# Kernel tuning notes

Measured on AMD Instinct MI355X. Metric: run time of the kernel, lower is better.

Reference implementation:

```python
import jax, jax.numpy as jnp
import numpy as np

K = 20  # kNN fan-out


def knn_idx(x, k):
    # x: (B, C, N). Negative squared pairwise distance; top-k largest = nearest.
    inner = -2.0 * jnp.einsum('bcn,bcm->bnm', x, x)        # (B, N, N)
    xx = jnp.sum(x * x, axis=1)                            # (B, N)
    pd = -xx[:, :, None] - inner - xx[:, None, :]          # (B, N, N)
    return jax.lax.top_k(pd, k)[1]                         # (B, N, k) int32


def get_graph_feature(x, k):
    # x: (B, C, N) -> edge features (B, 2C, N, k)
    idx = knn_idx(x, k)                                    # (B, N, k)
    xt = jnp.transpose(x, (0, 2, 1))                       # (B, N, C)
    nbrs = jax.vmap(lambda pts, ids: pts[ids])(xt, idx)    # (B, N, k, C)
    center = xt[:, :, None, :]                             # (B, N, 1, C)
    feat = jnp.concatenate(
        [nbrs - center, jnp.broadcast_to(center, nbrs.shape)], axis=-1)  # (B,N,k,2C)
    return jnp.transpose(feat, (0, 3, 1, 2))               # (B, 2C, N, k)


def vn_layer(W, x):
    # W: (out, in); x: (B, in, N, k) -> (B, out, N, k)
    return jnp.einsum('oi,bink->bonk', W, x)


def setup_inputs() -> dict:
    key = jax.random.key(0)
    ks = jax.random.split(key, 6)
    B, C, N = 16, 3, 2048
    num_classes = 10
    return {
        'x': jax.random.normal(ks[0], (B, C, N), dtype=jnp.float32),
        'W1': jax.random.normal(ks[1], (64, 6), dtype=jnp.float32),
        'W2': jax.random.normal(ks[2], (128, 64), dtype=jnp.float32),
        'W3': jax.random.normal(ks[3], (256, 128), dtype=jnp.float32),
        'fc_w': jax.random.normal(ks[4], (num_classes, 256), dtype=jnp.float32) * 0.0625,
        'fc_b': jax.random.normal(ks[5], (num_classes,), dtype=jnp.float32) * 0.0625,
    }


def reference(x, W1, W2, W3, fc_w, fc_b):
    h = get_graph_feature(x, K)          # (B, 6, N, k)
    h = vn_layer(W1, h)                  # (B, 64, N, k)
    h = jax.nn.relu(vn_layer(W2, h))     # (B, 128, N, k)
    h = jax.nn.relu(vn_layer(W3, h))     # (B, 256, N, k)
    h = jnp.max(h, axis=-1)              # max over neighbors k -> (B, 256, N)
    h = jnp.max(h, axis=-1)              # global max over points -> (B, 256)
    return h @ fc_w.T + fc_b             # (B, num_classes)
```

## Files before the change

### kernel.cpp

```cpp
#include <hip/hip_runtime.h>
#include <stdint.h>

typedef short v8s __attribute__((ext_vector_type(8)));
typedef float v4f __attribute__((ext_vector_type(4)));

#define NPTS 2048
#define BATCH 16
#define KNN 20
#define PAIRS (NPTS * KNN)

__device__ __forceinline__ unsigned bf16pack2(float lo, float hi) {
  unsigned ul = __float_as_uint(lo), uh = __float_as_uint(hi);
  return ((ul + 0x8000u) >> 16) | ((uh + 0x8000u) & 0xffff0000u);
}
__device__ __forceinline__ unsigned pair_h2(unsigned pu, unsigned qu) {
  float pl = __uint_as_float(pu << 16);
  float ph = __uint_as_float(pu & 0xffff0000u);
  float ql = __uint_as_float(qu << 16);
  float qh = __uint_as_float(qu & 0xffff0000u);
  return bf16pack2(fmaxf(pl + ql, 0.f), fmaxf(ph + qh, 0.f));
}

__global__ void prep_kernel(const float* __restrict__ W1, const float* __restrict__ W2,
                            float* __restrict__ M2a, float* __restrict__ M2b,
                            int* __restrict__ H) {
  if (blockIdx.x == 0 && threadIdx.x < 128) {
    int o = threadIdx.x;
    float a0 = 0, a1 = 0, a2 = 0, b0 = 0, b1 = 0, b2 = 0;
    for (int i = 0; i < 64; ++i) {
      float w2 = W2[o * 64 + i];
      const float* w1r = W1 + i * 6;
      a0 += w2 * w1r[0]; a1 += w2 * w1r[1]; a2 += w2 * w1r[2];
      b0 += w2 * (w1r[3] - w1r[0]); b1 += w2 * (w1r[4] - w1r[1]); b2 += w2 * (w1r[5] - w1r[2]);
    }
    M2a[o * 3 + 0] = a0; M2a[o * 3 + 1] = a1; M2a[o * 3 + 2] = a2;
    M2b[o * 3 + 0] = b0; M2b[o * 3 + 1] = b1; M2b[o * 3 + 2] = b2;
  }
  int g = blockIdx.x * 128 + threadIdx.x;
  if (g < BATCH * 256) H[g] = 0;
}

__global__ __launch_bounds__(64) void pq_kernel(const float* __restrict__ x,
                                                const float* __restrict__ M2a,
                                                const float* __restrict__ M2b,
                                                unsigned short* __restrict__ p,
                                                unsigned short* __restrict__ q) {
  int b = blockIdx.x >> 6;
  int j0 = (blockIdx.x & 63) << 5;
  int t = threadIdx.x;
  int o0 = t * 2;
  float a00 = M2a[o0 * 3 + 0], a01 = M2a[o0 * 3 + 1], a02 = M2a[o0 * 3 + 2];
  float a10 = M2a[o0 * 3 + 3], a11 = M2a[o0 * 3 + 4], a12 = M2a[o0 * 3 + 5];
  float b00 = M2b[o0 * 3 + 0], b01 = M2b[o0 * 3 + 1], b02 = M2b[o0 * 3 + 2];
  float b10 = M2b[o0 * 3 + 3], b11 = M2b[o0 * 3 + 4], b12 = M2b[o0 * 3 + 5];
  const float* xb = x + b * 3 * NPTS;
  unsigned* pw = (unsigned*)p;
  unsigned* qw = (unsigned*)q;
  for (int jj = 0; jj < 32; ++jj) {
    int j = j0 + jj;
    float x0 = xb[j], x1 = xb[NPTS + j], x2 = xb[2 * NPTS + j];
    float p0 = a00 * x0 + a01 * x1 + a02 * x2;
    float p1 = a10 * x0 + a11 * x1 + a12 * x2;
    float q0 = b00 * x0 + b01 * x1 + b02 * x2;
    float q1 = b10 * x0 + b11 * x1 + b12 * x2;
    size_t base = ((size_t)(b * NPTS + j)) * 64 + t;
    pw[base] = bf16pack2(p0, p1);
    qw[base] = bf16pack2(q0, q1);
  }
}

__global__ __launch_bounds__(256) void knn_kernel(const float* __restrict__ x,
                                                  int* __restrict__ idxOut) {
  __shared__ float px[NPTS], py[NPTS], pz[NPTS];
  __shared__ unsigned long long cand[4][4][128];
  int b = blockIdx.x >> 7;
  int qblk = blockIdx.x & 127;
  const float* xb = x + b * 3 * NPTS;
  for (int i = threadIdx.x; i < NPTS; i += 256) {
    px[i] = xb[i]; py[i] = xb[NPTS + i]; pz[i] = xb[2 * NPTS + i];
  }
  __syncthreads();
  int wid = threadIdx.x >> 6, lane = threadIdx.x & 63;
  int qbase = qblk * 16 + wid * 4;

  float qx[4], qy[4], qz[4], mn[4];
#pragma unroll
  for (int g = 0; g < 4; ++g) {
    qx[g] = px[qbase + g]; qy[g] = py[qbase + g]; qz[g] = pz[qbase + g];
    mn[g] = 1e30f;
  }

  for (int s = 0; s < 32; ++s) {
    int i = s * 64 + lane;
    float X = px[i], Y = py[i], Z = pz[i];
#pragma unroll
    for (int g = 0; g < 4; ++g) {
      float dx = X - qx[g], dy = Y - qy[g], dz = Z - qz[g];
      mn[g] = fminf(mn[g], dx * dx + dy * dy + dz * dz);
    }
  }

  float tau[4];
#pragma unroll
  for (int g = 0; g < 4; ++g) {
    float v = mn[g];
    for (int k = 2; k <= 64; k <<= 1) {
      for (int j = k >> 1; j > 0; j >>= 1) {
        float o = __shfl_xor(v, j);
        bool low = (lane & j) == 0;
        bool up = (lane & k) == 0;
        v = (low == up) ? fminf(v, o) : fmaxf(v, o);
      }
    }
    tau[g] = __shfl(v, 19) * (1.0f + 3.8e-6f);
  }

  int cnt[4] = {0, 0, 0, 0};
  for (int s = 0; s < 32; ++s) {
    int i = s * 64 + lane;
    float X = px[i], Y = py[i], Z = pz[i];
#pragma unroll
    for (int g = 0; g < 4; ++g) {
      float dx = X - qx[g], dy = Y - qy[g], dz = Z - qz[g];
      float d = dx * dx + dy * dy + dz * dz;
      bool take = d <= tau[g];
      unsigned long long mb = __ballot(take);
      if (take) {
        int pos = cnt[g] + __popcll(mb & ((1ull << lane) - 1ull));
        if (pos < 128)
          cand[wid][g][pos] =
              (((unsigned long long)__float_as_uint(d)) << 32) | (unsigned)i;
      }
      cnt[g] += __popcll(mb);
    }
  }

#pragma unroll
  for (int g = 0; g < 4; ++g) {
    int nc = cnt[g] < 128 ? cnt[g] : 128;
    unsigned long long k0 = (lane < nc) ? cand[wid][g][lane] : ~0ull;
    unsigned long long k1 = (lane + 64 < nc) ? cand[wid][g][lane + 64] : ~0ull;
    int r0 = 0, r1 = 0;
    for (int i = 0; i < nc; ++i) {
      unsigned long long ki = cand[wid][g][i];
      r0 += (ki < k0) ? 1 : 0;
      r1 += (ki < k1) ? 1 : 0;
    }
    long long obase = ((long long)b * NPTS + qbase + g) * KNN;
    if (lane < nc && r0 < KNN) idxOut[obase + r0] = (int)(k0 & 0xffffffffu);
    if (lane + 64 < nc && r1 < KNN) idxOut[obase + r1] = (int)(k1 & 0xffffffffu);
  }
}

__global__ __launch_bounds__(256, 2) void gemm_max_kernel(
    const unsigned short* __restrict__ p, const unsigned short* __restrict__ q,
    const int* __restrict__ idx, const float* __restrict__ W3, int* __restrict__ H) {
  __shared__ __align__(16) unsigned short h2s[2][16 * 136];

  int b = blockIdx.x & 15;
  int w = blockIdx.x >> 4;
  int t = threadIdx.x;
  int lane = t & 63, wid = t >> 6;
  int r16 = lane & 15, quad = lane >> 4;

  v8s bfr[4][4];
#pragma unroll
  for (int ntl = 0; ntl < 4; ++ntl) {
#pragma unroll
    for (int kk = 0; kk < 4; ++kk) {
      int n = (wid * 4 + ntl) * 16 + r16;
      const float* src = W3 + n * 128 + kk * 32 + quad * 8;
      v8s f;
#pragma unroll
      for (int jj = 0; jj < 8; ++jj)
        f[jj] = (short)((__float_as_uint(src[jj]) + 0x8000u) >> 16);
      bfr[ntl][kk] = f;
    }
  }

  const unsigned short* pB = p + (size_t)b * NPTS * 128;
  const unsigned short* qB = q + (size_t)b * NPTS * 128;
  const int* idxB = idx + (size_t)b * PAIRS;

  int pm = t >> 4;
  int cseg = t & 15;

  uint4 P4n, Q4n;
  {
    int pr = w * 16 + pm;
    int n0 = pr / 20;
    int j0 = idxB[pr] & (NPTS - 1);
    P4n = *(const uint4*)(pB + (size_t)j0 * 128 + cseg * 8);
    Q4n = *(const uint4*)(qB + (size_t)n0 * 128 + cseg * 8);
  }

  float vmx[4] = {0.f, 0.f, 0.f, 0.f};
  int buf = 0;
  for (int T = w; T < PAIRS / 16; T += 96) {
    uint4 R;
    R.x = pair_h2(P4n.x, Q4n.x);
    R.y = pair_h2(P4n.y, Q4n.y);
    R.z = pair_h2(P4n.z, Q4n.z);
    R.w = pair_h2(P4n.w, Q4n.w);
    *(uint4*)&h2s[buf][pm * 136 + cseg * 8] = R;
    __syncthreads();

    int Tn = T + 96;
    if (Tn < PAIRS / 16) {
      int prn = Tn * 16 + pm;
      int nn = prn / 20;
      int jn = idxB[prn] & (NPTS - 1);
      P4n = *(const uint4*)(pB + (size_t)jn * 128 + cseg * 8);
      Q4n = *(const uint4*)(qB + (size_t)nn * 128 + cseg * 8);
    }

    v8s a[4];
#pragma unroll
    for (int kk = 0; kk < 4; ++kk)
      a[kk] = *(const v8s*)&h2s[buf][r16 * 136 + kk * 32 + quad * 8];

#pragma unroll
    for (int ntl = 0; ntl < 4; ++ntl) {
      v4f acc = {0.f, 0.f, 0.f, 0.f};
#pragma unroll
      for (int kk = 0; kk < 4; ++kk)
        acc = __builtin_amdgcn_mfma_f32_16x16x32_bf16(a[kk], bfr[ntl][kk], acc, 0, 0, 0);
      vmx[ntl] = fmaxf(vmx[ntl], fmaxf(fmaxf(acc[0], acc[1]), fmaxf(acc[2], acc[3])));
    }
    buf ^= 1;
  }

#pragma unroll
  for (int ntl = 0; ntl < 4; ++ntl) {
    float vv = vmx[ntl];
    vv = fmaxf(vv, __shfl_xor(vv, 16));
    vv = fmaxf(vv, __shfl_xor(vv, 32));
    if (quad == 0) {
      int ch = (wid * 4 + ntl) * 16 + r16;
      atomicMax(&H[b * 256 + ch], __float_as_int(vv));
    }
  }
}

__global__ __launch_bounds__(64) void fc_kernel(const int* __restrict__ Hi,
                                                const float* __restrict__ fcw,
                                                const float* __restrict__ fcb,
                                                float* __restrict__ out) {
  int b = blockIdx.x / 10, r = blockIdx.x % 10;
  int lane = threadIdx.x;
  const float* Hb = (const float*)Hi + b * 256;
  float s = 0.f;
#pragma unroll
  for (int c = lane; c < 256; c += 64) s += Hb[c] * fcw[r * 256 + c];
#pragma unroll
  for (int m = 32; m > 0; m >>= 1) s += __shfl_xor(s, m);
  if (lane == 0) out[b * 10 + r] = s + fcb[r];
}

extern "C" void kernel_launch(void* const* d_in, const int* in_sizes, int n_in,
                              void* d_out, int out_size, void* d_ws, size_t ws_size,
                              hipStream_t stream) {
  const float* x   = (const float*)d_in[0];
  const float* W1  = (const float*)d_in[1];
  const float* W2  = (const float*)d_in[2];
  const float* W3  = (const float*)d_in[3];
  const float* fcw = (const float*)d_in[4];
  const float* fcb = (const float*)d_in[5];
  float* out = (float*)d_out;
  char* ws = (char*)d_ws;

  float* M2a = (float*)(ws + 0);
  float* M2b = (float*)(ws + 1536);
  int* H     = (int*)(ws + 4096);
  int* idx   = (int*)(ws + 24576);
  unsigned short* p = (unsigned short*)(ws + 3145728);
  unsigned short* q = (unsigned short*)(ws + 12582912);

  prep_kernel<<<32, 128, 0, stream>>>(W1, W2, M2a, M2b, H);
  pq_kernel<<<BATCH * 64, 64, 0, stream>>>(x, M2a, M2b, p, q);
  knn_kernel<<<BATCH * 128, 256, 0, stream>>>(x, idx);
  gemm_max_kernel<<<BATCH * 96, 256, 0, stream>>>(p, q, idx, W3, H);
  fc_kernel<<<BATCH * 10, 64, 0, stream>>>(H, fcw, fcb, out);
}
```

Measured before the change: 192.8 us.

## Build MFMA A-fragments in registers with fp16, drop LDS staging and barriers

```diff
diff --git a/kernel.cpp b/kernel.cpp
--- a/kernel.cpp
+++ b/kernel.cpp
@@ -1,7 +1,8 @@
 #include <hip/hip_runtime.h>
 #include <stdint.h>
 
-typedef short v8s __attribute__((ext_vector_type(8)));
+typedef _Float16 v8h __attribute__((ext_vector_type(8)));
+typedef _Float16 v2h __attribute__((ext_vector_type(2)));
 typedef float v4f __attribute__((ext_vector_type(4)));
 
 #define NPTS 2048
@@ -9,21 +10,40 @@
 #define KNN 20
 #define PAIRS (NPTS * KNN)
 
-__device__ __forceinline__ unsigned bf16pack2(float lo, float hi) {
-  unsigned ul = __float_as_uint(lo), uh = __float_as_uint(hi);
-  return ((ul + 0x8000u) >> 16) | ((uh + 0x8000u) & 0xffff0000u);
-}
-__device__ __forceinline__ unsigned pair_h2(unsigned pu, unsigned qu) {
-  float pl = __uint_as_float(pu << 16);
-  float ph = __uint_as_float(pu & 0xffff0000u);
-  float ql = __uint_as_float(qu << 16);
-  float qh = __uint_as_float(qu & 0xffff0000u);
-  return bf16pack2(fmaxf(pl + ql, 0.f), fmaxf(ph + qh, 0.f));
+__device__ __forceinline__ unsigned f2h2(float lo, float hi) {
+  _Float16 a = (_Float16)lo, b = (_Float16)hi;
+  unsigned short ua, ub;
+  __builtin_memcpy(&ua, &a, 2);
+  __builtin_memcpy(&ub, &b, 2);
+  return (unsigned)ua | ((unsigned)ub << 16);
+}
+__device__ __forceinline__ unsigned hadd_relu(unsigned a, unsigned b) {
+  v2h x, y;
+  __builtin_memcpy(&x, &a, 4);
+  __builtin_memcpy(&y, &b, 4);
+  v2h r = x + y;
+  v2h z = {(_Float16)0, (_Float16)0};
+  r = __builtin_elementwise_max(r, z);
+  unsigned o;
+  __builtin_memcpy(&o, &r, 4);
+  return o;
+}
+__device__ __forceinline__ v8h pack_a(uint4 P, uint4 Q) {
+  uint4 R;
+  R.x = hadd_relu(P.x, Q.x);
+  R.y = hadd_relu(P.y, Q.y);
+  R.z = hadd_relu(P.z, Q.z);
+  R.w = hadd_relu(P.w, Q.w);
+  v8h a;
+  __builtin_memcpy(&a, &R, 16);
+  return a;
 }
 
 __global__ void prep_kernel(const float* __restrict__ W1, const float* __restrict__ W2,
+                            const float* __restrict__ W3,
                             float* __restrict__ M2a, float* __restrict__ M2b,
-                            int* __restrict__ H) {
+                            unsigned short* __restrict__ W3h, int* __restrict__ H) {
+  int g = blockIdx.x * 128 + threadIdx.x;
   if (blockIdx.x == 0 && threadIdx.x < 128) {
     int o = threadIdx.x;
     float a0 = 0, a1 = 0, a2 = 0, b0 = 0, b1 = 0, b2 = 0;
@@ -36,7 +56,12 @@
     M2a[o * 3 + 0] = a0; M2a[o * 3 + 1] = a1; M2a[o * 3 + 2] = a2;
     M2b[o * 3 + 0] = b0; M2b[o * 3 + 1] = b1; M2b[o * 3 + 2] = b2;
   }
-  int g = blockIdx.x * 128 + threadIdx.x;
+  for (int i = g; i < 256 * 128; i += 4096) {
+    _Float16 h = (_Float16)W3[i];
+    unsigned short u;
+    __builtin_memcpy(&u, &h, 2);
+    W3h[i] = u;
+  }
   if (g < BATCH * 256) H[g] = 0;
 }
 
@@ -64,8 +89,8 @@
     float q0 = b00 * x0 + b01 * x1 + b02 * x2;
     float q1 = b10 * x0 + b11 * x1 + b12 * x2;
     size_t base = ((size_t)(b * NPTS + j)) * 64 + t;
-    pw[base] = bf16pack2(p0, p1);
-    qw[base] = bf16pack2(q0, q1);
+    pw[base] = f2h2(p0, p1);
+    qw[base] = f2h2(q0, q1);
   }
 }
 
@@ -134,7 +159,6 @@
       cnt[g] += __popcll(mb);
     }
   }
-
 #pragma unroll
   for (int g = 0; g < 4; ++g) {
     int nc = cnt[g] < 128 ? cnt[g] : 128;
@@ -152,82 +176,74 @@
   }
 }
 
-__global__ __launch_bounds__(256, 2) void gemm_max_kernel(
+__global__ __launch_bounds__(256, 3) void gemm_max_kernel(
     const unsigned short* __restrict__ p, const unsigned short* __restrict__ q,
-    const int* __restrict__ idx, const float* __restrict__ W3, int* __restrict__ H) {
-  __shared__ __align__(16) unsigned short h2s[2][16 * 136];
-
+    const int* __restrict__ idx, const unsigned short* __restrict__ W3h,
+    int* __restrict__ H) {
   int b = blockIdx.x & 15;
   int w = blockIdx.x >> 4;
   int t = threadIdx.x;
   int lane = t & 63, wid = t >> 6;
   int r16 = lane & 15, quad = lane >> 4;
 
-  v8s bfr[4][4];
+  v8h bfr[4][4];
 #pragma unroll
   for (int ntl = 0; ntl < 4; ++ntl) {
 #pragma unroll
     for (int kk = 0; kk < 4; ++kk) {
       int n = (wid * 4 + ntl) * 16 + r16;
-      const float* src = W3 + n * 128 + kk * 32 + quad * 8;
-      v8s f;
-#pragma unroll
-      for (int jj = 0; jj < 8; ++jj)
-        f[jj] = (short)((__float_as_uint(src[jj]) + 0x8000u) >> 16);
-      bfr[ntl][kk] = f;
-    }
-  }
-
-  const unsigned short* pB = p + (size_t)b * NPTS * 128;
-  const unsigned short* qB = q + (size_t)b * NPTS * 128;
+      bfr[ntl][kk] = *(const v8h*)(W3h + n * 128 + kk * 32 + quad * 8);
+    }
+  }
+
+  const char* pB = (const char*)p + (size_t)b * NPTS * 256;
+  const char* qB = (const char*)q + (size_t)b * NPTS * 256;
   const int* idxB = idx + (size_t)b * PAIRS;
 
-  int pm = t >> 4;
-  int cseg = t & 15;
-
-  uint4 P4n, Q4n;
+  int start = w * 53 + (w < 16 ? w : 16);
+  int cnt = 53 + (w < 16 ? 1 : 0);
+
+  uint4 P4[4], Q4[4];
   {
-    int pr = w * 16 + pm;
-    int n0 = pr / 20;
-    int j0 = idxB[pr] & (NPTS - 1);
-    P4n = *(const uint4*)(pB + (size_t)j0 * 128 + cseg * 8);
-    Q4n = *(const uint4*)(qB + (size_t)n0 * 128 + cseg * 8);
+    int pr = start * 16 + r16;
+    int j = idxB[pr] & (NPTS - 1);
+    unsigned n = (unsigned)pr / 20u;
+    const char* prow = pB + (size_t)j * 256 + quad * 16;
+    const char* qrow = qB + (size_t)n * 256 + quad * 16;
+#pragma unroll
+    for (int kk = 0; kk < 4; ++kk) {
+      P4[kk] = *(const uint4*)(prow + kk * 64);
+      Q4[kk] = *(const uint4*)(qrow + kk * 64);
+    }
   }
 
   float vmx[4] = {0.f, 0.f, 0.f, 0.f};
-  int buf = 0;
-  for (int T = w; T < PAIRS / 16; T += 96) {
-    uint4 R;
-    R.x = pair_h2(P4n.x, Q4n.x);
-    R.y = pair_h2(P4n.y, Q4n.y);
-    R.z = pair_h2(P4n.z, Q4n.z);
-    R.w = pair_h2(P4n.w, Q4n.w);
-    *(uint4*)&h2s[buf][pm * 136 + cseg * 8] = R;
-    __syncthreads();
-
-    int Tn = T + 96;
-    if (Tn < PAIRS / 16) {
-      int prn = Tn * 16 + pm;
-      int nn = prn / 20;
-      int jn = idxB[prn] & (NPTS - 1);
-      P4n = *(const uint4*)(pB + (size_t)jn * 128 + cseg * 8);
-      Q4n = *(const uint4*)(qB + (size_t)nn * 128 + cseg * 8);
-    }
-
-    v8s a[4];
-#pragma unroll
-    for (int kk = 0; kk < 4; ++kk)
-      a[kk] = *(const v8s*)&h2s[buf][r16 * 136 + kk * 32 + quad * 8];
+  for (int i = 0; i < cnt; ++i) {
+    v8h a[4];
+#pragma unroll
+    for (int kk = 0; kk < 4; ++kk) a[kk] = pack_a(P4[kk], Q4[kk]);
+
+    if (i + 1 < cnt) {
+      int pr = (start + i + 1) * 16 + r16;
+      int j = idxB[pr] & (NPTS - 1);
+      unsigned n = (unsigned)pr / 20u;
+      const char* prow = pB + (size_t)j * 256 + quad * 16;
+      const char* qrow = qB + (size_t)n * 256 + quad * 16;
+#pragma unroll
+      for (int kk = 0; kk < 4; ++kk) {
+        P4[kk] = *(const uint4*)(prow + kk * 64);
+        Q4[kk] = *(const uint4*)(qrow + kk * 64);
+      }
+    }
 
 #pragma unroll
     for (int ntl = 0; ntl < 4; ++ntl) {
       v4f acc = {0.f, 0.f, 0.f, 0.f};
 #pragma unroll
       for (int kk = 0; kk < 4; ++kk)
-        acc = __builtin_amdgcn_mfma_f32_16x16x32_bf16(a[kk], bfr[ntl][kk], acc, 0, 0, 0);
+        acc = __builtin_amdgcn_mfma_f32_16x16x32_f16(a[kk], bfr[ntl][kk], acc, 0, 0, 0);
       vmx[ntl] = fmaxf(vmx[ntl], fmaxf(fmaxf(acc[0], acc[1]), fmaxf(acc[2], acc[3])));
     }
-    buf ^= 1;
   }
 
 #pragma unroll
@@ -270,15 +286,16 @@
   char* ws = (char*)d_ws;
 
   float* M2a = (float*)(ws + 0);
-  float* M2b = (float*)(ws + 1536);
-  int* H     = (int*)(ws + 4096);
+  float* M2b = (float*)(ws + 2048);
+  int* H     = (int*)(ws + 8192);
   int* idx   = (int*)(ws + 24576);
-  unsigned short* p = (unsigned short*)(ws + 3145728);
-  unsigned short* q = (unsigned short*)(ws + 12582912);
-
-  prep_kernel<<<32, 128, 0, stream>>>(W1, W2, M2a, M2b, H);
+  unsigned short* W3h = (unsigned short*)(ws + 2646016);
+  unsigned short* p   = (unsigned short*)(ws + 2711552);
+  unsigned short* q   = (unsigned short*)(ws + 11100160);
+
+  prep_kernel<<<32, 128, 0, stream>>>(W1, W2, W3, M2a, M2b, W3h, H);
   pq_kernel<<<BATCH * 64, 64, 0, stream>>>(x, M2a, M2b, p, q);
   knn_kernel<<<BATCH * 128, 256, 0, stream>>>(x, idx);
-  gemm_max_kernel<<<BATCH * 96, 256, 0, stream>>>(p, q, idx, W3, H);
+  gemm_max_kernel<<<BATCH * 48, 256, 0, stream>>>(p, q, idx, W3h, H);
   fc_kernel<<<BATCH * 10, 64, 0, stream>>>(H, fcw, fcb, out);
 }
```

Measured after the change: 227.2 us. 17.8% more time.
